# Kernel optimization log

Measured on AMD Instinct MI355X. Metric: run time of the kernel, lower is better.

Reference implementation:

```python
import jax, jax.numpy as jnp
import numpy as np

EPS = 1e-5


def _gcn_conv(x, src, dst, n_nodes, W, b):
    # x: [N, Fin]; src/dst: [E+N] (self-loops already appended)
    h = x @ W                                   # [N, Fout]
    deg = jnp.zeros((n_nodes,), x.dtype).at[dst].add(1.0)
    dinv = jax.lax.rsqrt(deg)                   # deg >= 1 due to self-loops
    norm = dinv[src] * dinv[dst]                # [E+N]
    msg = h[src] * norm[:, None]                # [E+N, Fout]  (gather)
    out = jax.ops.segment_sum(msg, dst, num_segments=n_nodes)  # scatter-add
    return out + b


def _bn_relu(x, gamma, beta):
    # BatchNorm over nodes (training-style batch statistics), then ReLU.
    mu = jnp.mean(x, axis=0)
    var = jnp.mean((x - mu) ** 2, axis=0)       # biased variance (torch BN)
    xn = (x - mu) * jax.lax.rsqrt(var + EPS)
    return jax.nn.relu(xn * gamma + beta)


def setup_inputs() -> dict:
    key = jax.random.key(0)
    ks = jax.random.split(key, 12)
    N, E, Fin, H, O, G = 100000, 1600000, 128, 128, 64, 128
    x = jax.random.normal(ks[0], (N, Fin), dtype=jnp.float32)
    edge_index = jax.random.randint(ks[1], (2, E), 0, N, dtype=jnp.int64)
    batch = jnp.sort(jax.random.randint(ks[2], (N,), 0, G, dtype=jnp.int64))
    s = 1.0 / np.sqrt(Fin)
    W0 = jax.random.uniform(ks[3], (Fin, H), jnp.float32, -s, s)
    b0 = jnp.zeros((H,), jnp.float32)
    g0 = jnp.ones((H,), jnp.float32)
    be0 = jnp.zeros((H,), jnp.float32)
    s2 = 1.0 / np.sqrt(H)
    W1 = jax.random.uniform(ks[4], (H, H), jnp.float32, -s2, s2)
    b1 = jnp.zeros((H,), jnp.float32)
    g1 = jnp.ones((H,), jnp.float32)
    be1 = jnp.zeros((H,), jnp.float32)
    Wout = jax.random.uniform(ks[5], (H, O), jnp.float32, -s2, s2)
    bout = jax.random.uniform(ks[6], (O,), jnp.float32, -s2, s2)
    return {"x": x, "edge_index": edge_index, "batch": batch, "num_graphs": 128,
            "W0": W0, "b0": b0, "g0": g0, "be0": be0,
            "W1": W1, "b1": b1, "g1": g1, "be1": be1,
            "Wout": Wout, "bout": bout}


def reference(x, edge_index, batch, num_graphs,
              W0, b0, g0, be0, W1, b1, g1, be1, Wout, bout):
    N = x.shape[0]
    loops = jnp.arange(N, dtype=edge_index.dtype)
    src = jnp.concatenate([edge_index[0], loops])  # add self-loops
    dst = jnp.concatenate([edge_index[1], loops])
    h = _gcn_conv(x, src, dst, N, W0, b0)
    h = _bn_relu(h, g0, be0)                       # Dropout(p=0.1) = identity in eval
    h = _gcn_conv(h, src, dst, N, W1, b1)
    h = _bn_relu(h, g1, be1)
    # global mean pool over graphs
    sums = jax.ops.segment_sum(h, batch, num_segments=num_graphs)   # [G, H]
    cnt = jax.ops.segment_sum(jnp.ones((N,), h.dtype), batch, num_segments=num_graphs)
    pooled = sums / jnp.maximum(cnt, 1.0)[:, None]
    return pooled @ Wout + bout
```

## Files before the change

### kernel.cpp

```cpp
#include <hip/hip_runtime.h>
#include <hip/hip_bf16.h>

typedef _Float16 half8_t __attribute__((ext_vector_type(8)));
typedef _Float16 half4_t __attribute__((ext_vector_type(4)));
typedef _Float16 half2_t __attribute__((ext_vector_type(2)));
typedef float float4_t __attribute__((ext_vector_type(4)));


__global__ __launch_bounds__(256) void k_hist(const int* __restrict__ dst, int E, int SH,
                                              int NBK, int WG, int CH, int* __restrict__ M) {
    extern __shared__ int lh[];
    for (int i = threadIdx.x; i < NBK; i += 256) lh[i] = 0;
    __syncthreads();
    int wg = blockIdx.x;
    int e0 = wg * CH, e1 = min(E, e0 + CH);
    for (int e = e0 + threadIdx.x; e < e1; e += 256)
        atomicAdd(&lh[dst[e] >> SH], 1);
    __syncthreads();
    for (int i = threadIdx.x; i < NBK; i += 256) M[i * WG + wg] = lh[i];
}

__global__ __launch_bounds__(256) void k_colscan(int* __restrict__ M, int WG,
                                                 int* __restrict__ totals) {
    __shared__ int s[256];
    int b = blockIdx.x, t = threadIdx.x;
    int v = (t < WG) ? M[b * WG + t] : 0;
    s[t] = v;
    __syncthreads();
    for (int off = 1; off < 256; off <<= 1) {
        int u = (t >= off) ? s[t - off] : 0;
        __syncthreads();
        s[t] += u;
        __syncthreads();
    }
    if (t < WG) M[b * WG + t] = s[t] - v;
    if (t == 255) totals[b] = s[255];
}

__global__ __launch_bounds__(512) void k_bucketscan(const int* __restrict__ totals, int NBK,
                                                    int E, int* __restrict__ base) {
    __shared__ int s[512];
    int t = threadIdx.x;
    int v = (t < NBK) ? totals[t] : 0;
    s[t] = v;
    __syncthreads();
    for (int off = 1; off < 512; off <<= 1) {
        int u = (t >= off) ? s[t - off] : 0;
        __syncthreads();
        s[t] += u;
        __syncthreads();
    }
    if (t < NBK) base[t] = s[t] - v;
    if (t == 0) base[NBK] = E;
}

__global__ __launch_bounds__(256) void k_scatter(const int* __restrict__ src,
                                                 const int* __restrict__ dst, int E, int SH,
                                                 int NBK, int WG, int CH,
                                                 const int* __restrict__ M,
                                                 const int* __restrict__ base,
                                                 unsigned* __restrict__ ebuf,
                                                 int* __restrict__ slots, int N) {
    if (slots) {
        int4 f; f.x = N; f.y = N; f.z = N; f.w = N;
        int total4 = N * 8;
        for (int idx = blockIdx.x * 256 + threadIdx.x; idx < total4; idx += gridDim.x * 256)
            ((int4*)slots)[idx] = f;
    }
    extern __shared__ int cur[];
    int wg = blockIdx.x;
    for (int i = threadIdx.x; i < NBK; i += 256) cur[i] = base[i] + M[i * WG + wg];
    __syncthreads();
    int e0 = wg * CH, e1 = min(E, e0 + CH);
    for (int e = e0 + threadIdx.x; e < e1; e += 256) {
        int d = dst[e];
        int b = d >> SH;
        int pos = atomicAdd(&cur[b], 1);
        ebuf[pos] = (unsigned)src[e] | ((unsigned)(d - (b << SH)) << 23);
    }
}

__global__ __launch_bounds__(256) void k_cntfill(const unsigned* __restrict__ ebuf,
                                                 const int* __restrict__ base, int SH, int N,
                                                 int E, float* __restrict__ dinv,
                                                 int* __restrict__ rp, int* __restrict__ colx,
                                                 int* __restrict__ slots,
                                                 const float* __restrict__ W0,
                                                 const float* __restrict__ W1,
                                                 _Float16* __restrict__ Wt0,
                                                 _Float16* __restrict__ Wt1,
                                                 const int* __restrict__ batch, int G,
                                                 int* __restrict__ gptr,
                                                 float* __restrict__ psum,
                                                 float* __restrict__ sums,
                                                 unsigned char* __restrict__ A8) {
    __shared__ int h[512];
    __shared__ int cur[512];
    __shared__ int rs[512];
    __shared__ int lim[512];
    __shared__ int s[256];
    int b = blockIdx.x, t = threadIdx.x;

    if (b < 64) {
        int idx = b * 256 + t;
        int n = idx >> 7, k = idx & 127;
        Wt0[n * 128 + k] = (_Float16)W0[k * 128 + n];
        Wt1[n * 128 + k] = (_Float16)W1[k * 128 + n];
    } else if (b == 64) {
        if (t <= G) {
            int g = t;
            int lo = 0, hi = N;
            while (lo < hi) {
                int mid = (lo + hi) >> 1;
                if (batch[mid] < g) lo = mid + 1; else hi = mid;
            }
            gptr[g] = lo;
        }
    } else if (b < 97) {
        int i0 = (b - 65) * 512 + t;
        psum[i0] = 0.f;
        psum[i0 + 256] = 0.f;
    } else if (b == 97) {
        if (t < 256) { sums[t] = 0.f; sums[t + 256] = 0.f; }
        if (t < 32) ((unsigned*)A8)[(size_t)N * 32 + t] = 0u;
    }

    int n0 = b << SH;
    int nb = min(N - n0, 1 << SH);
    for (int i = t; i < nb; i += 256) h[i] = 0;
    __syncthreads();
    int e0 = base[b], e1 = base[b + 1];
    for (int e = e0 + t; e < e1; e += 256)
        atomicAdd(&h[ebuf[e] >> 23], 1);
    __syncthreads();
    int i0 = 2 * t, i1 = 2 * t + 1;
    int a0 = (i0 < nb) ? h[i0] : 0;
    int a1 = (i1 < nb) ? h[i1] : 0;
    int ps = a0 + a1;
    s[t] = ps;
    __syncthreads();
    for (int off = 1; off < 256; off <<= 1) {
        int u = (t >= off) ? s[t - off] : 0;
        __syncthreads();
        s[t] += u;
        __syncthreads();
    }
    int excl = s[t] - ps;
    if (i0 < nb) {
        int r0 = e0 + excl;
        cur[i0] = r0;
        rs[i0] = r0;
        lim[i0] = (a0 > 32) ? 31 : a0;
        rp[n0 + i0] = r0;
        dinv[n0 + i0] = rsqrtf((float)(a0 + 1));
        if (slots && a0 > 32) slots[(size_t)(n0 + i0) * 32 + 31] = 0x40000000 | r0;
    }
    if (i1 < nb) {
        int r1 = e0 + excl + a0;
        cur[i1] = r1;
        rs[i1] = r1;
        lim[i1] = (a1 > 32) ? 31 : a1;
        rp[n0 + i1] = r1;
        dinv[n0 + i1] = rsqrtf((float)(a1 + 1));
        if (slots && a1 > 32) slots[(size_t)(n0 + i1) * 32 + 31] = 0x40000000 | r1;
    }
    if (b == (int)gridDim.x - 1 && t == 0) rp[N] = E;
    __syncthreads();
    for (int e = e0 + t; e < e1; e += 256) {
        unsigned v = ebuf[e];
        int local = (int)(v >> 23);
        int srcn = (int)(v & 0x7FFFFFu);
        int pos = atomicAdd(&cur[local], 1);
        colx[pos] = srcn;
        if (slots) {
            int off = pos - rs[local];
            if (off < lim[local])
                slots[(size_t)(n0 + local) * 32 + off] = srcn;
        }
    }
}


__global__ __launch_bounds__(256) void k_gemmM(const float* __restrict__ X,
                                               const _Float16* __restrict__ Wt,
                                               const float* __restrict__ dinv,
                                               unsigned char* __restrict__ out, int N) {
    int t = threadIdx.x;
    int wv = t >> 6, lane = t & 63;
    int m = lane & 15, quad = lane >> 4;
    int rowbase = blockIdx.x * 64 + wv * 16;
    int arow = rowbase + m;
    int arowc = (arow < N) ? arow : (N - 1);
    const float* xr = X + (size_t)arowc * 128;

    float4_t acc[8];
    #pragma unroll
    for (int i = 0; i < 8; i++) acc[i] = (float4_t){0.f, 0.f, 0.f, 0.f};

    #pragma unroll
    for (int kc = 0; kc < 4; kc++) {
        int k0 = kc * 32 + quad * 8;
        float4 xa = *(const float4*)(xr + k0);
        float4 xb = *(const float4*)(xr + k0 + 4);
        float xv[8] = {xa.x, xa.y, xa.z, xa.w, xb.x, xb.y, xb.z, xb.w};
        half8_t a;
        #pragma unroll
        for (int j = 0; j < 8; j++) a[j] = (_Float16)xv[j];
        #pragma unroll
        for (int nt = 0; nt < 8; nt++) {
            half8_t b = *(const half8_t*)(Wt + (size_t)(nt * 16 + m) * 128 + k0);
            acc[nt] = __builtin_amdgcn_mfma_f32_16x16x32_f16(a, b, acc[nt], 0, 0, 0);
        }
    }

    float dv[4];
    #pragma unroll
    for (int r = 0; r < 4; r++) {
        int row = rowbase + quad * 4 + r;
        dv[r] = dinv[(row < N) ? row : (N - 1)];
    }
    #pragma unroll
    for (int r = 0; r < 4; r++) {
        int row = rowbase + quad * 4 + r;
        if (row < N) {
            unsigned char* o = out + (size_t)row * 128 + m;
            #pragma unroll
            for (int nt = 0; nt < 8; nt++) {
                float v = acc[nt][r] * dv[r];
                int pk = __builtin_amdgcn_cvt_pk_fp8_f32(v, v, 0, false);
                o[nt * 16] = (unsigned char)(pk & 0xFF);
            }
        }
    }
}

__global__ __launch_bounds__(256) void k_gemmM16(const _Float16* __restrict__ X,
                                                 const _Float16* __restrict__ Wt,
                                                 const float* __restrict__ sums,
                                                 const float* __restrict__ g,
                                                 const float* __restrict__ be,
                                                 const float* __restrict__ dinv,
                                                 unsigned char* __restrict__ out, int N) {
    __shared__ alignas(16) float ss[128];
    __shared__ alignas(16) float hh[128];
    int t = threadIdx.x;
    if (t < 128) {
        float invN = 1.0f / (float)N;
        float mu = sums[t] * invN;
        float var = fmaxf(sums[128 + t] * invN - mu * mu, 0.f);
        float sc = g[t] * rsqrtf(var + 1e-5f);
        ss[t] = sc;
        hh[t] = fmaf(-mu, sc, be[t]);
    }
    __syncthreads();

    int wv = t >> 6, lane = t & 63;
    int m = lane & 15, quad = lane >> 4;
    int rowbase = blockIdx.x * 64 + wv * 16;
    int arow = rowbase + m;
    int arowc = (arow < N) ? arow : (N - 1);
    const _Float16* xr = X + (size_t)arowc * 128;

    float4_t acc[8];
    #pragma unroll
    for (int i = 0; i < 8; i++) acc[i] = (float4_t){0.f, 0.f, 0.f, 0.f};

    #pragma unroll
    for (int kc = 0; kc < 4; kc++) {
        int k0 = kc * 32 + quad * 8;
        half8_t x8 = *(const half8_t*)(xr + k0);
        float4 sa = *(const float4*)(ss + k0);
        float4 sb = *(const float4*)(ss + k0 + 4);
        float4 ha = *(const float4*)(hh + k0);
        float4 hb = *(const float4*)(hh + k0 + 4);
        float sv[8] = {sa.x, sa.y, sa.z, sa.w, sb.x, sb.y, sb.z, sb.w};
        float hv[8] = {ha.x, ha.y, ha.z, ha.w, hb.x, hb.y, hb.z, hb.w};
        half8_t a;
        #pragma unroll
        for (int j = 0; j < 8; j++)
            a[j] = (_Float16)fmaxf(fmaf((float)x8[j], sv[j], hv[j]), 0.f);
        #pragma unroll
        for (int nt = 0; nt < 8; nt++) {
            half8_t b = *(const half8_t*)(Wt + (size_t)(nt * 16 + m) * 128 + k0);
            acc[nt] = __builtin_amdgcn_mfma_f32_16x16x32_f16(a, b, acc[nt], 0, 0, 0);
        }
    }

    float dv[4];
    #pragma unroll
    for (int r = 0; r < 4; r++) {
        int row = rowbase + quad * 4 + r;
        dv[r] = dinv[(row < N) ? row : (N - 1)];
    }
    #pragma unroll
    for (int r = 0; r < 4; r++) {
        int row = rowbase + quad * 4 + r;
        if (row < N) {
            unsigned char* o = out + (size_t)row * 128 + m;
            #pragma unroll
            for (int nt = 0; nt < 8; nt++) {
                float v = acc[nt][r] * dv[r];
                int pk = __builtin_amdgcn_cvt_pk_fp8_f32(v, v, 0, false);
                o[nt * 16] = (unsigned char)(pk & 0xFF);
            }
        }
    }
}


__device__ __forceinline__ void f8x4(unsigned w, float* o) {
    o[0] = __builtin_amdgcn_cvt_f32_fp8((int)w, 0);
    o[1] = __builtin_amdgcn_cvt_f32_fp8((int)w, 1);
    o[2] = __builtin_amdgcn_cvt_f32_fp8((int)w, 2);
    o[3] = __builtin_amdgcn_cvt_f32_fp8((int)w, 3);
}

__global__ __launch_bounds__(256) void k_aggS8(const unsigned char* __restrict__ hs,
                                               const int* __restrict__ slots,
                                               const int* __restrict__ rp,
                                               const int* __restrict__ colx,
                                               const float* __restrict__ dinv,
                                               const float* __restrict__ bias,
                                               _Float16* __restrict__ out, int N) {
    int wave = (blockIdx.x * 256 + threadIdx.x) >> 6;
    int lane = threadIdx.x & 63;
    if (wave >= N) return;
    int i = wave;
    int q = lane >> 4;
    int c8 = lane & 15;

    const int4* sl4 = (const int4*)(slots + (size_t)i * 32 + 8 * q);
    int4 sa = sl4[0];
    int4 sb = sl4[1];
    int last = slots[(size_t)i * 32 + 31];
    uint2 sw = *(const uint2*)(hs + (size_t)i * 128 + c8 * 8);

    bool ovf = ((unsigned)last & 0x40000000u) != 0;
    int j[8] = {sa.x, sa.y, sa.z, sa.w, sb.x, sb.y, sb.z, sb.w};
    if (ovf && q == 3) j[7] = N;

    uint2 v[8];
    #pragma unroll
    for (int s2 = 0; s2 < 8; s2++)
        v[s2] = *(const uint2*)(hs + (size_t)j[s2] * 128 + c8 * 8);

    float a[8] = {0.f, 0.f, 0.f, 0.f, 0.f, 0.f, 0.f, 0.f};
    #pragma unroll
    for (int s2 = 0; s2 < 8; s2++) {
        float f0[4], f1[4];
        f8x4(v[s2].x, f0);
        f8x4(v[s2].y, f1);
        #pragma unroll
        for (int b = 0; b < 4; b++) { a[b] += f0[b]; a[4 + b] += f1[b]; }
    }

    if (ovf) {
        int k0 = last & 0x3FFFFFFF;
        int k1 = rp[i + 1];
        for (int k = k0 + 31 + q; k < k1; k += 4) {
            uint2 vv = *(const uint2*)(hs + (size_t)colx[k] * 128 + c8 * 8);
            float f0[4], f1[4];
            f8x4(vv.x, f0);
            f8x4(vv.y, f1);
            #pragma unroll
            for (int b = 0; b < 4; b++) { a[b] += f0[b]; a[4 + b] += f1[b]; }
        }
    }

    #pragma unroll
    for (int t = 0; t < 8; t++) {
        float x = a[t];
        x += __shfl_xor(x, 16);
        x += __shfl_xor(x, 32);
        a[t] = x;
    }

    if (q == 0) {
        float d = dinv[i];
        float4 bA = ((const float4*)bias)[2 * c8];
        float4 bB = ((const float4*)bias)[2 * c8 + 1];
        float bb[8] = {bA.x, bA.y, bA.z, bA.w, bB.x, bB.y, bB.z, bB.w};
        float sf[8];
        f8x4(sw.x, sf);
        f8x4(sw.y, sf + 4);
        half8_t o;
        #pragma unroll
        for (int t = 0; t < 8; t++)
            o[t] = (_Float16)fmaf(a[t] + sf[t], d, bb[t]);
        ((half8_t*)out)[(size_t)i * 16 + c8] = o;
    }
}

__global__ __launch_bounds__(256) void k_aggC8(const unsigned char* __restrict__ hs,
                                               const int* __restrict__ rp,
                                               const int* __restrict__ colx,
                                               const float* __restrict__ dinv,
                                               const float* __restrict__ bias,
                                               _Float16* __restrict__ out, int N) {
    int wave = (blockIdx.x * 256 + threadIdx.x) >> 6;
    int lane = threadIdx.x & 63;
    if (wave >= N) return;
    int i = wave;
    int q = lane >> 4;
    int c8 = lane & 15;

    uint2 sw = *(const uint2*)(hs + (size_t)i * 128 + c8 * 8);
    int k0 = rp[i], k1 = rp[i + 1];

    float a[8] = {0.f, 0.f, 0.f, 0.f, 0.f, 0.f, 0.f, 0.f};
    for (int k = k0 + q; k < k1; k += 4) {
        uint2 vv = *(const uint2*)(hs + (size_t)colx[k] * 128 + c8 * 8);
        float f0[4], f1[4];
        f8x4(vv.x, f0);
        f8x4(vv.y, f1);
        #pragma unroll
        for (int b = 0; b < 4; b++) { a[b] += f0[b]; a[4 + b] += f1[b]; }
    }

    #pragma unroll
    for (int t = 0; t < 8; t++) {
        float x = a[t];
        x += __shfl_xor(x, 16);
        x += __shfl_xor(x, 32);
        a[t] = x;
    }

    if (q == 0) {
        float d = dinv[i];
        float4 bA = ((const float4*)bias)[2 * c8];
        float4 bB = ((const float4*)bias)[2 * c8 + 1];
        float bb[8] = {bA.x, bA.y, bA.z, bA.w, bB.x, bB.y, bB.z, bB.w};
        float sf[8];
        f8x4(sw.x, sf);
        f8x4(sw.y, sf + 4);
        half8_t o;
        #pragma unroll
        for (int t = 0; t < 8; t++)
            o[t] = (_Float16)fmaf(a[t] + sf[t], d, bb[t]);
        ((half8_t*)out)[(size_t)i * 16 + c8] = o;
    }
}


__global__ __launch_bounds__(256) void k_stats(const _Float16* __restrict__ x, int N,
                                               float* __restrict__ sums) {
    int lane = threadIdx.x & 63;
    int wv = threadIdx.x >> 6;
    int gw = blockIdx.x * 4 + wv;
    int stride = gridDim.x * 4;
    const half2_t* b = (const half2_t*)x;
    float2 s = make_float2(0.f, 0.f), q = make_float2(0.f, 0.f);
    for (int i = gw; i < N; i += stride) {
        half2_t v = b[(size_t)i * 64 + lane];
        float vx = (float)v.x, vy = (float)v.y;
        s.x += vx; s.y += vy;
        q.x += vx * vx; q.y += vy * vy;
    }
    __shared__ float ls[4][128];
    __shared__ float lq[4][128];
    ls[wv][2 * lane] = s.x; ls[wv][2 * lane + 1] = s.y;
    lq[wv][2 * lane] = q.x; lq[wv][2 * lane + 1] = q.y;
    __syncthreads();
    int t = threadIdx.x;
    if (t < 128) {
        float ts = ls[0][t] + ls[1][t] + ls[2][t] + ls[3][t];
        float tq = lq[0][t] + lq[1][t] + lq[2][t] + lq[3][t];
        atomicAdd(&sums[t], ts);
        atomicAdd(&sums[128 + t], tq);
    }
}


__global__ __launch_bounds__(256) void k_pool2(const _Float16* __restrict__ x,
                                               const int* __restrict__ batch,
                                               const float* __restrict__ sums,
                                               const float* __restrict__ g2,
                                               const float* __restrict__ be2,
                                               float* __restrict__ psum, int N) {
    __shared__ alignas(8) float ss[128];
    __shared__ alignas(8) float hh[128];
    int t = threadIdx.x;
    if (t < 128) {
        float invN = 1.0f / (float)N;
        float mu = sums[t] * invN;
        float var = fmaxf(sums[128 + t] * invN - mu * mu, 0.f);
        float sc = g2[t] * rsqrtf(var + 1e-5f);
        ss[t] = sc;
        hh[t] = fmaf(-mu, sc, be2[t]);
    }
    __syncthreads();

    int nw = gridDim.x * 4;
    int w = blockIdx.x * 4 + (threadIdx.x >> 6);
    int lane = threadIdx.x & 63;
    int per = (N + nw - 1) / nw;
    int i0 = w * per, i1 = min(N, i0 + per);
    if (i0 >= i1) return;
    const half2_t* b = (const half2_t*)x;
    float2 s2 = ((const float2*)ss)[lane];
    float2 h2 = ((const float2*)hh)[lane];
    float2 acc = make_float2(0.f, 0.f);
    int g = batch[i0];
    for (int i = i0; i < i1; i++) {
        int gi = batch[i];
        if (gi != g) {
            atomicAdd(&psum[g * 128 + 2 * lane], acc.x);
            atomicAdd(&psum[g * 128 + 2 * lane + 1], acc.y);
            acc = make_float2(0.f, 0.f);
            g = gi;
        }
        half2_t v = b[(size_t)i * 64 + lane];
        acc.x += fmaxf(fmaf((float)v.x, s2.x, h2.x), 0.f);
        acc.y += fmaxf(fmaf((float)v.y, s2.y, h2.y), 0.f);
    }
    atomicAdd(&psum[g * 128 + 2 * lane], acc.x);
    atomicAdd(&psum[g * 128 + 2 * lane + 1], acc.y);
}


__global__ __launch_bounds__(64) void k_final(const float* __restrict__ psum,
                                              const int* __restrict__ gptr,
                                              const float* __restrict__ Wout,
                                              const float* __restrict__ bout,
                                              float* __restrict__ out, int O) {
    int g = blockIdx.x, o = threadIdx.x;
    int cnt = gptr[g + 1] - gptr[g];
    float inv = 1.0f / fmaxf((float)cnt, 1.f);
    float acc = 0.f;
    for (int c = 0; c < 128; c++) acc = fmaf(psum[g * 128 + c], Wout[c * O + o], acc);
    out[g * O + o] = fmaf(acc, inv, bout[o]);
}


extern "C" void kernel_launch(void* const* d_in, const int* in_sizes, int n_in,
                              void* d_out, int out_size, void* d_ws, size_t ws_size,
                              hipStream_t stream) {
    const float* x    = (const float*)d_in[0];
    const int*   edge = (const int*)d_in[1];
    const int*   batch= (const int*)d_in[2];
    const float* W0   = (const float*)d_in[4];
    const float* b0   = (const float*)d_in[5];
    const float* g0   = (const float*)d_in[6];
    const float* be0  = (const float*)d_in[7];
    const float* W1   = (const float*)d_in[8];
    const float* b1   = (const float*)d_in[9];
    const float* g1   = (const float*)d_in[10];
    const float* be1  = (const float*)d_in[11];
    const float* Wout = (const float*)d_in[12];
    const float* bout = (const float*)d_in[13];
    float* out = (float*)d_out;

    const int Hh  = in_sizes[5];
    const int Fin = in_sizes[4] / Hh;
    const int N   = in_sizes[0] / Fin;
    const int E   = in_sizes[1] / 2;
    const int O   = in_sizes[13];
    const int G   = out_size / O;
    (void)Hh; (void)n_in;

    int SH = 8;
    while (((N + (1 << SH) - 1) >> SH) > 512) SH++;
    const int NBK = (N + (1 << SH) - 1) >> SH;
    const int CH  = ((E + 255) / 256 > 8192) ? (E + 255) / 256 : 8192;
    const int WG  = (E + CH - 1) / CH;

    char* p = (char*)d_ws;
    auto alloc = [&](size_t bytes) -> void* {
        void* r = (void*)p;
        p += (bytes + 255) & ~(size_t)255;
        return r;
    };
    unsigned char* A8 = (unsigned char*)alloc((size_t)(N + 1) * 128);
    _Float16* B   = (_Float16*)alloc((size_t)(N + 1) * 128 * 2);
    float* dinv   = (float*)alloc((size_t)N * 4);
    int*   rp     = (int*)alloc((size_t)(N + 1) * 4);
    int*   colx   = (int*)alloc((size_t)E * 4);
    unsigned* ebuf= (unsigned*)alloc((size_t)E * 4);
    int*   M      = (int*)alloc((size_t)NBK * WG * 4);
    int*   totals = (int*)alloc((size_t)NBK * 4);
    int*   base   = (int*)alloc((size_t)(NBK + 1) * 4);
    float* sums   = (float*)alloc(512 * 4);
    int*   gptr   = (int*)alloc((size_t)(G + 1) * 4);
    float* psum   = (float*)alloc((size_t)G * 128 * 4);
    _Float16* Wt0 = (_Float16*)alloc(128 * 128 * 2);
    _Float16* Wt1 = (_Float16*)alloc(128 * 128 * 2);
    int*   slots  = (int*)alloc((size_t)N * 32 * 4);
    bool useSlots = ((size_t)(p - (char*)d_ws) <= ws_size);
    if (!useSlots) slots = nullptr;

    const int* src = edge;
    const int* dst = edge + E;

    k_hist<<<WG, 256, NBK * 4, stream>>>(dst, E, SH, NBK, WG, CH, M);
    k_colscan<<<NBK, 256, 0, stream>>>(M, WG, totals);
    k_bucketscan<<<1, 512, 0, stream>>>(totals, NBK, E, base);
    k_scatter<<<WG, 256, NBK * 4, stream>>>(src, dst, E, SH, NBK, WG, CH, M, base, ebuf,
                                            slots, N);
    k_cntfill<<<NBK, 256, 0, stream>>>(ebuf, base, SH, N, E, dinv, rp, colx, slots,
                                       W0, W1, Wt0, Wt1, batch, G, gptr, psum, sums, A8);

    k_gemmM<<<(N + 63) / 64, 256, 0, stream>>>(x, Wt0, dinv, A8, N);
    if (useSlots)
        k_aggS8<<<(N + 3) / 4, 256, 0, stream>>>(A8, slots, rp, colx, dinv, b0, B, N);
    else
        k_aggC8<<<(N + 3) / 4, 256, 0, stream>>>(A8, rp, colx, dinv, b0, B, N);
    k_stats<<<512, 256, 0, stream>>>(B, N, sums);

    k_gemmM16<<<(N + 63) / 64, 256, 0, stream>>>(B, Wt1, sums, g0, be0, dinv, A8, N);
    if (useSlots)
        k_aggS8<<<(N + 3) / 4, 256, 0, stream>>>(A8, slots, rp, colx, dinv, b1, B, N);
    else
        k_aggC8<<<(N + 3) / 4, 256, 0, stream>>>(A8, rp, colx, dinv, b1, B, N);
    k_stats<<<512, 256, 0, stream>>>(B, N, sums + 256);

    k_pool2<<<512, 256, 0, stream>>>(B, batch, sums + 256, g1, be1, psum, N);
    k_final<<<G, 64, 0, stream>>>(psum, gptr, Wout, bout, out, O);
}
```

Baseline: 410.6 us.

## Interleave neighbor slot layout, skip unused slot loads, use packed fp8 conversion

Slot entries are now stored interleaved so each quarter-wave's first 4 loads cover the first 16 neighbors, and the second group of slots is read only when degree exceeds 16. The overflow sentinel is replaced by reading row pointers directly, and all 32 slots are filled before falling back to the column list. Accumulation switches to packed fp8-to-float2 conversion with vector adds. The intent is fewer wasted gathers for low-degree nodes and fewer conversion instructions, at the cost of an extra rp load and a data-dependent branch.

```diff
diff --git a/kernel.cpp b/kernel.cpp
--- a/kernel.cpp
+++ b/kernel.cpp
@@ -5,6 +5,7 @@
 typedef _Float16 half4_t __attribute__((ext_vector_type(4)));
 typedef _Float16 half2_t __attribute__((ext_vector_type(2)));
 typedef float float4_t __attribute__((ext_vector_type(4)));
+typedef float float2_t __attribute__((ext_vector_type(2)));
 
 
 __global__ __launch_bounds__(256) void k_hist(const int* __restrict__ dst, int E, int SH,
@@ -150,19 +151,17 @@
         int r0 = e0 + excl;
         cur[i0] = r0;
         rs[i0] = r0;
-        lim[i0] = (a0 > 32) ? 31 : a0;
+        lim[i0] = min(a0, 32);
         rp[n0 + i0] = r0;
         dinv[n0 + i0] = rsqrtf((float)(a0 + 1));
-        if (slots && a0 > 32) slots[(size_t)(n0 + i0) * 32 + 31] = 0x40000000 | r0;
     }
     if (i1 < nb) {
         int r1 = e0 + excl + a0;
         cur[i1] = r1;
         rs[i1] = r1;
-        lim[i1] = (a1 > 32) ? 31 : a1;
+        lim[i1] = min(a1, 32);
         rp[n0 + i1] = r1;
         dinv[n0 + i1] = rsqrtf((float)(a1 + 1));
-        if (slots && a1 > 32) slots[(size_t)(n0 + i1) * 32 + 31] = 0x40000000 | r1;
     }
     if (b == (int)gridDim.x - 1 && t == 0) rp[N] = E;
     __syncthreads();
@@ -174,8 +173,10 @@
         colx[pos] = srcn;
         if (slots) {
             int off = pos - rs[local];
-            if (off < lim[local])
-                slots[(size_t)(n0 + local) * 32 + off] = srcn;
+            if (off < lim[local]) {
+                int idx = ((off & 3) << 3) + (off >> 2);
+                slots[(size_t)(n0 + local) * 32 + idx] = srcn;
+            }
         }
     }
 }
@@ -308,6 +309,13 @@
 }
 
 
+__device__ __forceinline__ void acc8(uint2 v, float2_t* a2) {
+    a2[0] += __builtin_amdgcn_cvt_pk_f32_fp8((int)v.x, false);
+    a2[1] += __builtin_amdgcn_cvt_pk_f32_fp8((int)v.x, true);
+    a2[2] += __builtin_amdgcn_cvt_pk_f32_fp8((int)v.y, false);
+    a2[3] += __builtin_amdgcn_cvt_pk_f32_fp8((int)v.y, true);
+}
+
 __device__ __forceinline__ void f8x4(unsigned w, float* o) {
     o[0] = __builtin_amdgcn_cvt_f32_fp8((int)w, 0);
     o[1] = __builtin_amdgcn_cvt_f32_fp8((int)w, 1);
@@ -331,42 +339,40 @@
 
     const int4* sl4 = (const int4*)(slots + (size_t)i * 32 + 8 * q);
     int4 sa = sl4[0];
-    int4 sb = sl4[1];
-    int last = slots[(size_t)i * 32 + 31];
+    int k0 = rp[i], k1 = rp[i + 1];
     uint2 sw = *(const uint2*)(hs + (size_t)i * 128 + c8 * 8);
-
-    bool ovf = ((unsigned)last & 0x40000000u) != 0;
-    int j[8] = {sa.x, sa.y, sa.z, sa.w, sb.x, sb.y, sb.z, sb.w};
-    if (ovf && q == 3) j[7] = N;
-
-    uint2 v[8];
-    #pragma unroll
-    for (int s2 = 0; s2 < 8; s2++)
-        v[s2] = *(const uint2*)(hs + (size_t)j[s2] * 128 + c8 * 8);
-
-    float a[8] = {0.f, 0.f, 0.f, 0.f, 0.f, 0.f, 0.f, 0.f};
-    #pragma unroll
-    for (int s2 = 0; s2 < 8; s2++) {
-        float f0[4], f1[4];
-        f8x4(v[s2].x, f0);
-        f8x4(v[s2].y, f1);
-        #pragma unroll
-        for (int b = 0; b < 4; b++) { a[b] += f0[b]; a[4 + b] += f1[b]; }
-    }
-
-    if (ovf) {
-        int k0 = last & 0x3FFFFFFF;
-        int k1 = rp[i + 1];
-        for (int k = k0 + 31 + q; k < k1; k += 4) {
-            uint2 vv = *(const uint2*)(hs + (size_t)colx[k] * 128 + c8 * 8);
-            float f0[4], f1[4];
-            f8x4(vv.x, f0);
-            f8x4(vv.y, f1);
-            #pragma unroll
-            for (int b = 0; b < 4; b++) { a[b] += f0[b]; a[4 + b] += f1[b]; }
-        }
-    }
-
+    int deg = k1 - k0;
+
+    float2_t a2[4] = {{0.f, 0.f}, {0.f, 0.f}, {0.f, 0.f}, {0.f, 0.f}};
+
+    {
+        int ja[4] = {sa.x, sa.y, sa.z, sa.w};
+        uint2 v[4];
+        #pragma unroll
+        for (int s = 0; s < 4; s++)
+            v[s] = *(const uint2*)(hs + (size_t)ja[s] * 128 + c8 * 8);
+        #pragma unroll
+        for (int s = 0; s < 4; s++) acc8(v[s], a2);
+    }
+    if (deg > 16) {
+        int4 sb = sl4[1];
+        int jb[4] = {sb.x, sb.y, sb.z, sb.w};
+        uint2 v[4];
+        #pragma unroll
+        for (int s = 0; s < 4; s++)
+            v[s] = *(const uint2*)(hs + (size_t)jb[s] * 128 + c8 * 8);
+        #pragma unroll
+        for (int s = 0; s < 4; s++) acc8(v[s], a2);
+        if (deg > 32) {
+            for (int k = k0 + 32 + q; k < k1; k += 4) {
+                uint2 vv = *(const uint2*)(hs + (size_t)colx[k] * 128 + c8 * 8);
+                acc8(vv, a2);
+            }
+        }
+    }
+
+    float a[8] = {a2[0].x, a2[0].y, a2[1].x, a2[1].y,
+                  a2[2].x, a2[2].y, a2[3].x, a2[3].y};
     #pragma unroll
     for (int t = 0; t < 8; t++) {
         float x = a[t];
@@ -407,16 +413,14 @@
     uint2 sw = *(const uint2*)(hs + (size_t)i * 128 + c8 * 8);
     int k0 = rp[i], k1 = rp[i + 1];
 
-    float a[8] = {0.f, 0.f, 0.f, 0.f, 0.f, 0.f, 0.f, 0.f};
+    float2_t a2[4] = {{0.f, 0.f}, {0.f, 0.f}, {0.f, 0.f}, {0.f, 0.f}};
     for (int k = k0 + q; k < k1; k += 4) {
         uint2 vv = *(const uint2*)(hs + (size_t)colx[k] * 128 + c8 * 8);
-        float f0[4], f1[4];
-        f8x4(vv.x, f0);
-        f8x4(vv.y, f1);
-        #pragma unroll
-        for (int b = 0; b < 4; b++) { a[b] += f0[b]; a[4 + b] += f1[b]; }
-    }
-
+        acc8(vv, a2);
+    }
+
+    float a[8] = {a2[0].x, a2[0].y, a2[1].x, a2[1].y,
+                  a2[2].x, a2[2].y, a2[3].x, a2[3].y};
     #pragma unroll
     for (int t = 0; t < 8; t++) {
         float x = a[t];
```

Result: faster. 401.6 us (-2.2%).
